# Optimization experiments

Hardware: AMD Instinct MI355X
Metric: run time of the kernel (lower is better)

Reference implementation:

```python
import jax, jax.numpy as jnp
import numpy as np

# config (matches init_kwargs)
B, H, N, D = 2, 8, 2048, 64
ALPHA = 1.0        # < 2 -> power-law kernel branch
D_INT = 4.0        # d_intrinsic
BW = 1.0           # bandwidth
A = 0.5            # dual-sided degree-normalization exponent
R = 1.0            # sphere_radius
MASK_VAL = 10000.0
EPS = 1e-7


def setup_inputs() -> dict:
    key = jax.random.key(0)
    k1, k2, k3, k4 = jax.random.split(key, 4)
    Q = jax.random.normal(k1, (B, H, N, D), dtype=jnp.float32)
    K = jax.random.normal(k2, (B, H, N, D), dtype=jnp.float32)
    V = jax.random.normal(k3, (B, H, N, D), dtype=jnp.float32)
    mask = jax.random.randint(k4, (B, N), 0, 2).astype(jnp.int32)
    return {"Q": Q, "K": K, "V": V, "mask": mask}


def reference(Q, K, V, mask) -> jnp.ndarray:
    # geodesic distance on the sphere: acos(clamp(QK^T)) * radius  [B,H,N,N]
    qk = jnp.einsum('bhnd,bhmd->bhnm', Q, K)
    g_dist = jnp.arccos(jnp.clip(qk, -1.0 + EPS, 1.0 - EPS)) * R
    # key-side padding mask: [B,N] -> [B,1,1,N]
    g_dist = jnp.where(mask[:, None, None, :] == 0, MASK_VAL, g_dist)
    # power-law kernel (alpha < 2 branch)
    attn_score = (1.0 + g_dist / jnp.sqrt(BW)) ** (-D_INT - ALPHA)
    # dual-sided degree normalization (a != 0 branch)
    n_r = jnp.sum(attn_score, axis=-1)   # row degrees [B,H,N]
    n_c = jnp.sum(attn_score, axis=-2)   # col degrees [B,H,N]
    k_tilde = (n_r ** (-A))[..., :, None] * attn_score * (n_c ** (-A))[..., None, :]
    # F.normalize(p=1, dim=3)
    attn = k_tilde / jnp.maximum(jnp.sum(jnp.abs(k_tilde), axis=-1, keepdims=True), 1e-12)
    # dropout p=0.0 -> identity
    return jnp.einsum('bhnm,bhmd->bhnd', attn, V)
```

## Files before the change

kernel.cpp:

```cpp
#include <hip/hip_runtime.h>
#include <hip/hip_bf16.h>
#include <math.h>

#define B_ 2
#define H_ 8
#define N_ 2048
#define D_ 64
#define BH_ 16
#define NT_ (N_/64)
#define LS 72
#define LSW (LS/2)

typedef __attribute__((ext_vector_type(8))) short short8;
typedef __attribute__((ext_vector_type(4))) float float4v;
typedef __attribute__((ext_vector_type(2))) float float2v;

__device__ __forceinline__ float2v splat2(float s){ float2v v; v.x=s; v.y=s; return v; }

__device__ __forceinline__ unsigned packbf2(float a, float b){
  __hip_bfloat162 h = __float22bfloat162_rn(make_float2(a, b));
  return *(unsigned*)&h;
}
__device__ __forceinline__ void split2(float a, float b, unsigned& hi, unsigned& lo){
  hi = packbf2(a, b);
  float ha = __uint_as_float(hi << 16);
  float hb = __uint_as_float(hi & 0xFFFF0000u);
  lo = packbf2(a - ha, b - hb);
}
__device__ __forceinline__ void load_split8(const float* p, short8& hi8, short8& lo8){
  float4v v0 = *(const float4v*)p;
  float4v v1 = *(const float4v*)(p + 4);
  unsigned h0,h1,h2,h3,l0,l1,l2,l3;
  split2(v0.x, v0.y, h0, l0);
  split2(v0.z, v0.w, h1, l1);
  split2(v1.x, v1.y, h2, l2);
  split2(v1.z, v1.w, h3, l3);
  unsigned ph[4] = {h0,h1,h2,h3};
  unsigned pl[4] = {l0,l1,l2,l3};
  hi8 = *(short8*)ph;
  lo8 = *(short8*)pl;
}

__device__ __forceinline__ float2v score2(float2v qk){
  float2v ax;
  ax.x = fminf(fabsf(qk.x), 1.0f - 1e-7f);
  ax.y = fminf(fabsf(qk.y), 1.0f - 1e-7f);
  float2v p = __builtin_elementwise_fma(
                __builtin_elementwise_fma(
                  __builtin_elementwise_fma(splat2(-0.0187293f), ax, splat2(0.0742610f)),
                  ax, splat2(-0.2121144f)),
                ax, splat2(1.5707288f));
  float2v u = __builtin_elementwise_fma(ax, splat2(-1.0f), splat2(1.0f));
  float2v t;
  t.x = __builtin_amdgcn_sqrtf(u.x);
  t.y = __builtin_amdgcn_sqrtf(u.y);
  float2v t2 = t * p;
  float2v gn = __builtin_elementwise_fma(t2, splat2(-1.0f), splat2(3.14159265358979f));
  float2v g;
  g.x = (qk.x >= 0.0f) ? t2.x : gn.x;
  g.y = (qk.y >= 0.0f) ? t2.y : gn.y;
  float2v w1 = g + splat2(1.0f);
  float2v w2 = w1 * w1;
  float2v w4 = w2 * w2;
  float2v w5 = w4 * w1;
  float2v r;
  r.x = __builtin_amdgcn_rcpf(w5.x);
  r.y = __builtin_amdgcn_rcpf(w5.y);
  return r;
}

__device__ __forceinline__ float score_fn_m(float qk, float masked){
  float ax = fminf(fabsf(qk), 1.0f - 1e-7f);
  float t  = __builtin_amdgcn_sqrtf(1.0f - ax);
  float p  = __builtin_fmaf(__builtin_fmaf(__builtin_fmaf(-0.0187293f, ax, 0.0742610f),
                                           ax, -0.2121144f), ax, 1.5707288f);
  float t2 = t * p;
  float g  = (qk >= 0.0f) ? t2 : (3.14159265358979f - t2);
  g = (masked != 0.0f) ? 10000.0f : g;
  float w1 = 1.0f + g;
  float w2 = w1*w1;
  float w4 = w2*w2;
  return __builtin_amdgcn_rcpf(w4*w1);
}

__global__ __launch_bounds__(256) void k0_split(
    const float* __restrict__ Q, const float* __restrict__ K,
    unsigned short* __restrict__ Qh, unsigned short* __restrict__ Ql,
    unsigned short* __restrict__ Kh, unsigned short* __restrict__ Kl)
{
  size_t i = (size_t)blockIdx.x*256 + threadIdx.x;
  const size_t tot = (size_t)BH_*N_*D_/8;
  const float* src; unsigned short *dh, *dl;
  if (i < tot){ src = Q; dh = Qh; dl = Ql; }
  else        { src = K; dh = Kh; dl = Kl; i -= tot; }
  short8 hi, lo;
  load_split8(src + i*8, hi, lo);
  *(short8*)&dh[i*8] = hi;
  *(short8*)&dl[i*8] = lo;
}

template<bool PRE>
__global__ __launch_bounds__(256) void k1_score(
    const float* __restrict__ Qf, const float* __restrict__ Kf,
    const unsigned short* __restrict__ Qh, const unsigned short* __restrict__ Ql,
    const unsigned short* __restrict__ Kh, const unsigned short* __restrict__ Kl,
    float* __restrict__ ncw, unsigned short* __restrict__ S)
{
  __shared__ float red[64*4];
  const int id = blockIdx.x;
  const int xcd = id & 7;
  const int r0 = id >> 3;
  const int kt = r0 & 31;
  const int grp = r0 >> 5;
  const int flat = grp*8 + xcd;
  const int bh = flat & 15;
  const int rz = flat >> 4;
  const int nz = 4;
  const int tid = threadIdx.x;
  const int wv = tid>>6, lane = tid&63, quad = lane>>4, l15 = lane&15;

  short8 khi[4][2], klo[4][2];
  if constexpr (PRE){
    #pragma unroll
    for (int s=0;s<4;++s){
      const size_t r = (size_t)(bh*N_ + kt*64 + s*16 + l15)*D_ + quad*8;
      khi[s][0] = *(const short8*)&Kh[r];
      khi[s][1] = *(const short8*)&Kh[r+32];
      klo[s][0] = *(const short8*)&Kl[r];
      klo[s][1] = *(const short8*)&Kl[r+32];
    }
  } else {
    #pragma unroll
    for (int s=0;s<4;++s){
      const float* kp = Kf + (size_t)(bh*N_ + kt*64 + s*16 + l15)*D_ + quad*8;
      load_split8(kp,      khi[s][0], klo[s][0]);
      load_split8(kp + 32, khi[s][1], klo[s][1]);
    }
  }

  float2v cs2[4][2];
  #pragma unroll
  for (int s=0;s<4;++s){ cs2[s][0] = splat2(0.f); cs2[s][1] = splat2(0.f); }

  const int iters = NT_/nz;
  const int rt0 = rz*iters;

  const size_t qoff0 = (size_t)(bh*N_ + rt0*64 + wv*16 + l15)*D_ + quad*8;
  const unsigned lconst = (unsigned)(((quad>>1)<<7) + (l15<<3) + ((quad&1)<<2));
  unsigned short* Sp = S + ((((size_t)(bh*NT_ + kt)*NT_ + rt0)*4 + wv)<<10) + lconst;

  short8 qh0,qh1,ql0,ql1;
  if constexpr (PRE){
    const unsigned short* qp = Qh + qoff0;
    const unsigned short* lp = Ql + qoff0;
    qh0 = *(const short8*)qp;      qh1 = *(const short8*)(qp+32);
    ql0 = *(const short8*)lp;      ql1 = *(const short8*)(lp+32);
  } else {
    const float* qp = Qf + qoff0;
    load_split8(qp,      qh0, ql0);
    load_split8(qp + 32, qh1, ql1);
  }

  for (int rti=0; rti<iters; ++rti){
    short8 nh0,nh1,nl0,nl1;
    const size_t qoffn = qoff0 + (size_t)(rti + ((rti+1<iters) ? 1 : 0))*4096;
    if constexpr (PRE){
      const unsigned short* qp = Qh + qoffn;
      const unsigned short* lp = Ql + qoffn;
      nh0 = *(const short8*)qp;    nh1 = *(const short8*)(qp+32);
      nl0 = *(const short8*)lp;    nl1 = *(const short8*)(lp+32);
    } else {
      const float* qp = Qf + qoffn;
      load_split8(qp,      nh0, nl0);
      load_split8(qp + 32, nh1, nl1);
    }

    #pragma unroll
    for (int s=0;s<4;++s){
      float4v c = {0.f,0.f,0.f,0.f};
      c = __builtin_amdgcn_mfma_f32_16x16x32_bf16(khi[s][0], qh0, c, 0,0,0);
      c = __builtin_amdgcn_mfma_f32_16x16x32_bf16(khi[s][0], ql0, c, 0,0,0);
      c = __builtin_amdgcn_mfma_f32_16x16x32_bf16(klo[s][0], qh0, c, 0,0,0);
      c = __builtin_amdgcn_mfma_f32_16x16x32_bf16(khi[s][1], qh1, c, 0,0,0);
      c = __builtin_amdgcn_mfma_f32_16x16x32_bf16(khi[s][1], ql1, c, 0,0,0);
      c = __builtin_amdgcn_mfma_f32_16x16x32_bf16(klo[s][1], qh1, c, 0,0,0);
      float2v c01; c01.x = c[0]; c01.y = c[1];
      float2v c23; c23.x = c[2]; c23.y = c[3];
      float2v s01 = score2(c01);
      float2v s23 = score2(c23);
      cs2[s][0] += s01;
      cs2[s][1] += s23;
      uint2 pk;
      pk.x = packbf2(s01.x, s01.y);
      pk.y = packbf2(s23.x, s23.y);
      *(uint2*)(Sp + (s<<8)) = pk;
    }
    Sp += 4096;
    qh0=nh0; qh1=nh1; ql0=nl0; ql1=nl1;
  }

  float cs[4][4];
  #pragma unroll
  for (int s=0;s<4;++s){
    cs[s][0]=cs2[s][0].x; cs[s][1]=cs2[s][0].y;
    cs[s][2]=cs2[s][1].x; cs[s][3]=cs2[s][1].y;
  }

  #pragma unroll
  for (int s=0;s<4;++s)
    #pragma unroll
    for (int i=0;i<4;++i){
      float v2 = cs[s][i];
      v2 += __shfl_xor(v2, 1);
      v2 += __shfl_xor(v2, 2);
      v2 += __shfl_xor(v2, 4);
      v2 += __shfl_xor(v2, 8);
      cs[s][i] = v2;
    }
  if (l15 == 0){
    #pragma unroll
    for (int s=0;s<4;++s)
      #pragma unroll
      for (int i=0;i<4;++i)
        red[(s*16 + quad*4 + i)*4 + wv] = cs[s][i];
  }
  __syncthreads();
  if (tid < 64){
    float t = red[tid*4+0] + red[tid*4+1] + red[tid*4+2] + red[tid*4+3];
    atomicAdd(&ncw[bh*N_ + kt*64 + tid], t);
  }
}

__global__ __launch_bounds__(256) void k2_pack(
    const float* __restrict__ V, const float* __restrict__ nc,
    const int* __restrict__ mask, unsigned short* __restrict__ Vw)
{
  __shared__ float T[64*65];
  __shared__ float wrow[64];
  const int mt = blockIdx.x, bh = blockIdx.y;
  const int tid = threadIdx.x;
  const float* Vg = V + (size_t)bh*N_*D_;
  const float* ncg = nc + (size_t)bh*N_;
  unsigned short* Fb = Vw + ((size_t)(bh*NT_ + mt)*10)*512;

  {
    int m = tid >> 2;
    int d0 = (tid & 3) * 16;
    int gm = mt*64 + m;
    float wm = (mask[(bh>>3)*N_ + gm] == 0) ? 0.0f
             : (1.0f / sqrtf(fmaxf(ncg[gm], 1e-30f)));
    if (d0 == 0) wrow[m] = wm;
    #pragma unroll
    for (int j=0;j<4;++j){
      float4v v = *(const float4v*)(Vg + (size_t)gm*D_ + d0 + j*4);
      T[(d0+j*4+0)*65 + m] = v.x*wm;
      T[(d0+j*4+1)*65 + m] = v.y*wm;
      T[(d0+j*4+2)*65 + m] = v.z*wm;
      T[(d0+j*4+3)*65 + m] = v.w*wm;
    }
  }
  __syncthreads();

  for (int idx = tid; idx < 640; idx += 256){
    int f = idx >> 6, lane = idx & 63;
    int quad = lane >> 4, l15 = lane & 15;
    int s2 = f >> 1, cc = f & 1;
    int m0 = cc*32 + quad*8;
    unsigned pk[4];
    if (s2 < 4){
      int d = s2*16 + l15;
      #pragma unroll
      for (int j=0;j<4;++j)
        pk[j] = packbf2(T[d*65 + m0 + 2*j], T[d*65 + m0 + 2*j + 1]);
    } else if (l15 == 0){
      #pragma unroll
      for (int j=0;j<4;++j)
        pk[j] = packbf2(wrow[m0 + 2*j], wrow[m0 + 2*j + 1]);
    } else {
      pk[0]=pk[1]=pk[2]=pk[3]=0u;
    }
    *(short8*)(Fb + ((size_t)f*64 + lane)*8) = *(short8*)pk;
  }
}

__global__ __launch_bounds__(512) void k3_direct(
    const unsigned short* __restrict__ S, const unsigned short* __restrict__ Vw,
    float* __restrict__ out)
{
  __shared__ float Red[64*68];

  const int id = blockIdx.x;
  const int xcd = id & 7;
  const int r0 = id >> 3;
  const int rt = r0 & 31;
  const int bhh = r0 >> 5;
  const int bh = bhh*8 + xcd;

  const int tid = threadIdx.x;
  const int wvid = tid >> 6;
  const int g    = wvid >> 2;
  const int slot = wvid & 3;
  const int lane = tid & 63, quad = lane >> 4, l15 = lane & 15;
  const int row = rt*64 + slot*16 + l15;

  const size_t sb0 = ((((size_t)bh*NT_ + g*16)*NT_ + rt)*4 + (size_t)slot)*1024
                   + (size_t)quad*128 + (size_t)l15*8;
  const unsigned short* Vb = Vw + ((size_t)(bh*NT_ + g*16)*10)*512 + (size_t)lane*8;

  float4v acc[4];
  #pragma unroll
  for (int i=0;i<4;++i) acc[i] = (float4v){0.f,0.f,0.f,0.f};
  float4v c5 = {0.f,0.f,0.f,0.f};

  short8 sA0 = *(const short8*)&S[sb0];
  short8 sA1 = *(const short8*)&S[sb0 + 512];
  short8 sB0 = *(const short8*)&S[sb0 + 131072];
  short8 sB1 = *(const short8*)&S[sb0 + 131072 + 512];

  #pragma unroll 1
  for (int k2 = 0; k2 < 8; ++k2){
    const int ktA = k2*2, ktB = k2*2 + 1;
    {
      const unsigned short* Vp = Vb + (size_t)ktA*5120;
      short8 va[10];
      #pragma unroll
      for (int f=0; f<10; ++f)
        va[f] = *(const short8*)(Vp + (size_t)f*512);
      short8 p0 = sA0, p1 = sA1;
      if (ktA + 2 < 16){
        const size_t sb = sb0 + (size_t)(ktA+2)*131072;
        sA0 = *(const short8*)&S[sb];
        sA1 = *(const short8*)&S[sb + 512];
      }
      #pragma unroll
      for (int s2=0;s2<4;++s2){
        acc[s2] = __builtin_amdgcn_mfma_f32_16x16x32_bf16(va[s2*2+0], p0, acc[s2], 0,0,0);
        acc[s2] = __builtin_amdgcn_mfma_f32_16x16x32_bf16(va[s2*2+1], p1, acc[s2], 0,0,0);
      }
      c5 = __builtin_amdgcn_mfma_f32_16x16x32_bf16(va[8], p0, c5, 0,0,0);
      c5 = __builtin_amdgcn_mfma_f32_16x16x32_bf16(va[9], p1, c5, 0,0,0);
    }
    {
      const unsigned short* Vp = Vb + (size_t)ktB*5120;
      short8 va[10];
      #pragma unroll
      for (int f=0; f<10; ++f)
        va[f] = *(const short8*)(Vp + (size_t)f*512);
      short8 p0 = sB0, p1 = sB1;
      if (ktB + 2 < 16){
        const size_t sb = sb0 + (size_t)(ktB+2)*131072;
        sB0 = *(const short8*)&S[sb];
        sB1 = *(const short8*)&S[sb + 512];
      }
      #pragma unroll
      for (int s2=0;s2<4;++s2){
        acc[s2] = __builtin_amdgcn_mfma_f32_16x16x32_bf16(va[s2*2+0], p0, acc[s2], 0,0,0);
        acc[s2] = __builtin_amdgcn_mfma_f32_16x16x32_bf16(va[s2*2+1], p1, acc[s2], 0,0,0);
      }
      c5 = __builtin_amdgcn_mfma_f32_16x16x32_bf16(va[8], p0, c5, 0,0,0);
      c5 = __builtin_amdgcn_mfma_f32_16x16x32_bf16(va[9], p1, c5, 0,0,0);
    }
  }

  if (g == 1){
    float* Rr = Red + (size_t)(slot*16 + l15)*68;
    #pragma unroll
    for (int s2=0;s2<4;++s2)
      #pragma unroll
      for (int i=0;i<4;++i)
        Rr[s2*16 + quad*4 + i] = acc[s2][i];
    if (quad == 0) Rr[64] = c5[0];
  }
  __syncthreads();
  if (g == 0){
    const float* Rr = Red + (size_t)(slot*16 + l15)*68;
    #pragma unroll
    for (int s2=0;s2<4;++s2)
      #pragma unroll
      for (int i=0;i<4;++i)
        acc[s2][i] += Rr[s2*16 + quad*4 + i];
    float rs = __shfl(c5[0], l15) + Rr[64];
    float inv = 1.0f / fmaxf(rs, 1e-12f);

    float* Og = out + (size_t)bh*N_*D_ + (size_t)row*D_;
    #pragma unroll
    for (int s2=0;s2<4;++s2)
      #pragma unroll
      for (int i=0;i<4;++i)
        Og[s2*16 + quad*4 + i] = acc[s2][i] * inv;
  }
}

__global__ __launch_bounds__(256) void k1_fallback(
    const float* __restrict__ Q, const float* __restrict__ K,
    const int* __restrict__ mask, float* __restrict__ ncw)
{
  __shared__ float msk[64];
  __shared__ float red[64*4];
  const int kt = blockIdx.x, bh = blockIdx.y;
  const int tid = threadIdx.x;
  const int wv = tid>>6, lane = tid&63, quad = lane>>4, l15 = lane&15;

  const float* Qg = Q + (size_t)bh*N_*D_;
  const float* Kg = K + (size_t)bh*N_*D_;

  short8 khi[4][2], klo[4][2];
  #pragma unroll
  for (int s=0;s<4;++s){
    const float* kp = Kg + (size_t)(kt*64 + s*16 + l15)*D_ + quad*8;
    load_split8(kp,      khi[s][0], klo[s][0]);
    load_split8(kp + 32, khi[s][1], klo[s][1]);
  }
  if (tid < 64)
    msk[tid] = (mask[(bh>>3)*N_ + kt*64 + tid] == 0) ? 1.f : 0.f;
  __syncthreads();

  float cs[4][4];
  #pragma unroll
  for (int s=0;s<4;++s)
    #pragma unroll
    for (int i=0;i<4;++i) cs[s][i] = 0.f;

  for (int rt=0; rt<NT_; ++rt){
    const float* qp = Qg + (size_t)(rt*64 + wv*16 + l15)*D_ + quad*8;
    short8 bhi[2], blo[2];
    load_split8(qp,      bhi[0], blo[0]);
    load_split8(qp + 32, bhi[1], blo[1]);

    #pragma unroll
    for (int s=0;s<4;++s){
      float4v c = {0.f,0.f,0.f,0.f};
      #pragma unroll
      for (int cc=0; cc<2; ++cc){
        c = __builtin_amdgcn_mfma_f32_16x16x32_bf16(khi[s][cc], bhi[cc], c, 0,0,0);
        c = __builtin_amdgcn_mfma_f32_16x16x32_bf16(khi[s][cc], blo[cc], c, 0,0,0);
        c = __builtin_amdgcn_mfma_f32_16x16x32_bf16(klo[s][cc], bhi[cc], c, 0,0,0);
      }
      int kl = s*16 + quad*4;
      cs[s][0] += score_fn_m(c[0], msk[kl+0]);
      cs[s][1] += score_fn_m(c[1], msk[kl+1]);
      cs[s][2] += score_fn_m(c[2], msk[kl+2]);
      cs[s][3] += score_fn_m(c[3], msk[kl+3]);
    }
  }

  #pragma unroll
  for (int s=0;s<4;++s)
    #pragma unroll
    for (int i=0;i<4;++i){
      float v2 = cs[s][i];
      v2 += __shfl_xor(v2, 1);
      v2 += __shfl_xor(v2, 2);
      v2 += __shfl_xor(v2, 4);
      v2 += __shfl_xor(v2, 8);
      cs[s][i] = v2;
    }
  if (l15 == 0){
    #pragma unroll
    for (int s=0;s<4;++s)
      #pragma unroll
      for (int i=0;i<4;++i)
        red[(s*16 + quad*4 + i)*4 + wv] = cs[s][i];
  }
  __syncthreads();
  if (tid < 64){
    float t = red[tid*4+0] + red[tid*4+1] + red[tid*4+2] + red[tid*4+3];
    ncw[bh*N_ + kt*64 + tid] = 1.0f / sqrtf(t);
  }
}

__global__ __launch_bounds__(256) void spop_pass2(
    const float* __restrict__ Q, const float* __restrict__ K,
    const float* __restrict__ V, const int* __restrict__ mask,
    const float* __restrict__ w, float* __restrict__ out)
{
  __shared__ unsigned short Khi[64*LS], Klo[64*LS];
  __shared__ unsigned short Vt[64*LS];
  __shared__ unsigned short Ps[64*LS];
  __shared__ float msk[64], wms[64];

  const int rt = blockIdx.x, bh = blockIdx.y, b = bh>>3;
  const int tid = threadIdx.x;
  const int wv = tid>>6, lane = tid&63, quad = lane>>4, l15 = lane&15;

  const float* Qg = Q + (size_t)bh*N_*D_;
  const float* Kg = K + (size_t)bh*N_*D_;
  const float* Vg = V + (size_t)bh*N_*D_;

  short8 qhi[2], qlo[2];
  {
    const float* qp = Qg + (size_t)(rt*64 + wv*16 + l15)*D_ + quad*8;
    load_split8(qp,      qhi[0], qlo[0]);
    load_split8(qp + 32, qhi[1], qlo[1]);
  }

  float4v acc[4];
  #pragma unroll
  for (int i=0;i<4;++i) acc[i] = (float4v){0.f,0.f,0.f,0.f};
  float rs = 0.f;

  for (int kt=0; kt<NT_; ++kt){
    __syncthreads();
    #pragma unroll
    for (int it=0; it<4; ++it){
      int idx = tid + it*256;
      int r = idx>>4, d4 = (idx&15)<<2;
      const float4v v = *(const float4v*)(Kg + (size_t)(kt*64 + r)*D_ + d4);
      unsigned h0,l0,h1,l1;
      split2(v.x, v.y, h0, l0);
      split2(v.z, v.w, h1, l1);
      unsigned* KhiW = (unsigned*)Khi; unsigned* KloW = (unsigned*)Klo;
      int base = r*LSW + (d4>>1);
      KhiW[base] = h0; KhiW[base+1] = h1;
      KloW[base] = l0; KloW[base+1] = l1;
    }
    #pragma unroll
    for (int it=0; it<2; ++it){
      int u = tid + it*256;
      int kp = u & 31;
      int d4 = (u>>5)<<2;
      const float* vp = Vg + (size_t)(kt*64 + kp*2)*D_ + d4;
      float4v a0 = *(const float4v*)vp;
      float4v a1 = *(const float4v*)(vp + D_);
      unsigned* VtW = (unsigned*)Vt;
      VtW[(d4+0)*LSW + kp] = packbf2(a0.x, a1.x);
      VtW[(d4+1)*LSW + kp] = packbf2(a0.y, a1.y);
      VtW[(d4+2)*LSW + kp] = packbf2(a0.z, a1.z);
      VtW[(d4+3)*LSW + kp] = packbf2(a0.w, a1.w);
    }
    if (tid < 64){
      int gk = kt*64 + tid;
      msk[tid] = (mask[b*N_ + gk] == 0) ? 1.f : 0.f;
      wms[tid] = w[bh*N_ + gk];
    }
    __syncthreads();

    #pragma unroll
    for (int s=0;s<4;++s){
      float4v c = {0.f,0.f,0.f,0.f};
      #pragma unroll
      for (int cc=0; cc<2; ++cc){
        const short8 ahi = *(const short8*)&Khi[(s*16+l15)*LS + cc*32 + quad*8];
        const short8 alo = *(const short8*)&Klo[(s*16+l15)*LS + cc*32 + quad*8];
        c = __builtin_amdgcn_mfma_f32_16x16x32_bf16(ahi, qhi[cc], c, 0,0,0);
        c = __builtin_amdgcn_mfma_f32_16x16x32_bf16(ahi, qlo[cc], c, 0,0,0);
        c = __builtin_amdgcn_mfma_f32_16x16x32_bf16(alo, qhi[cc], c, 0,0,0);
      }
      int kl = s*16 + quad*4;
      float sc0 = score_fn_m(c[0], msk[kl+0]) * wms[kl+0];
      float sc1 = score_fn_m(c[1], msk[kl+1]) * wms[kl+1];
      float sc2 = score_fn_m(c[2], msk[kl+2]) * wms[kl+2];
      float sc3 = score_fn_m(c[3], msk[kl+3]) * wms[kl+3];
      rs += (sc0 + sc1) + (sc2 + sc3);
      unsigned* PsW = (unsigned*)Ps;
      int pb = (wv*16 + l15)*LSW + (kl>>1);
      PsW[pb]   = packbf2(sc0, sc1);
      PsW[pb+1] = packbf2(sc2, sc3);
    }

    short8 pf[2];
    pf[0] = *(const short8*)&Ps[(wv*16+l15)*LS +  0 + quad*8];
    pf[1] = *(const short8*)&Ps[(wv*16+l15)*LS + 32 + quad*8];
    #pragma unroll
    for (int s2=0;s2<4;++s2){
      #pragma unroll
      for (int cc=0; cc<2; ++cc){
        const short8 av = *(const short8*)&Vt[(s2*16+l15)*LS + cc*32 + quad*8];
        acc[s2] = __builtin_amdgcn_mfma_f32_16x16x32_bf16(av, pf[cc], acc[s2], 0,0,0);
      }
    }
  }

  rs += __shfl_xor(rs, 16);
  rs += __shfl_xor(rs, 32);
  float inv = 1.0f / fmaxf(rs, 1e-12f);

  float* Og = out + (size_t)bh*N_*D_ + (size_t)(rt*64 + wv*16 + l15)*D_;
  #pragma unroll
  for (int s2=0;s2<4;++s2)
    #pragma unroll
    for (int i=0;i<4;++i)
      Og[s2*16 + quad*4 + i] = acc[s2][i] * inv;
}

extern "C" void kernel_launch(void* const* d_in, const int* in_sizes, int n_in,
                              void* d_out, int out_size, void* d_ws, size_t ws_size,
                              hipStream_t stream) {
  (void)in_sizes; (void)n_in; (void)out_size;
  const float* Q   = (const float*)d_in[0];
  const float* K   = (const float*)d_in[1];
  const float* V   = (const float*)d_in[2];
  const int*  mask = (const int*)d_in[3];
  float* out = (float*)d_out;

  const size_t nc_bytes = (size_t)BH_*N_*sizeof(float);
  const size_t vw_off   = 131072;
  const size_t vw_bytes = (size_t)BH_*NT_*10*512*2;
  const size_t qk_off   = vw_off + vw_bytes;
  const size_t qk_one   = (size_t)BH_*N_*D_;
  const size_t qk_bytes = 4*qk_one*2;
  const size_t S_bytes  = (size_t)2*BH_*N_*N_;
  const size_t need_A   = qk_off + qk_bytes + S_bytes;
  const size_t need_B   = qk_off + S_bytes;

  if (ws_size >= need_A){
    float* nc = (float*)d_ws;
    unsigned short* Vw = (unsigned short*)((char*)d_ws + vw_off);
    unsigned short* Qh = (unsigned short*)((char*)d_ws + qk_off);
    unsigned short* Ql = Qh + qk_one;
    unsigned short* Kh = Ql + qk_one;
    unsigned short* Kl = Kh + qk_one;
    unsigned short* S  = (unsigned short*)((char*)d_ws + qk_off + qk_bytes);
    hipMemsetAsync(nc, 0, nc_bytes, stream);
    k0_split<<<dim3(2048), 256, 0, stream>>>(Q, K, Qh, Ql, Kh, Kl);
    k1_score<true><<<dim3(2048), 256, 0, stream>>>(
        nullptr, nullptr, Qh, Ql, Kh, Kl, nc, S);
    k2_pack<<<dim3(NT_, BH_), 256, 0, stream>>>(V, nc, mask, Vw);
    k3_direct<<<dim3(512), 512, 0, stream>>>(S, Vw, out);
  } else if (ws_size >= need_B){
    float* nc = (float*)d_ws;
    unsigned short* Vw = (unsigned short*)((char*)d_ws + vw_off);
    unsigned short* S  = (unsigned short*)((char*)d_ws + qk_off);
    hipMemsetAsync(nc, 0, nc_bytes, stream);
    k1_score<false><<<dim3(2048), 256, 0, stream>>>(
        Q, K, nullptr, nullptr, nullptr, nullptr, nc, S);
    k2_pack<<<dim3(NT_, BH_), 256, 0, stream>>>(V, nc, mask, Vw);
    k3_direct<<<dim3(512), 512, 0, stream>>>(S, Vw, out);
  } else {
    float* w = (float*)d_ws;
    k1_fallback<<<dim3(NT_, BH_), 256, 0, stream>>>(Q, K, mask, w);
    spop_pass2<<<dim3(NT_, BH_), 256, 0, stream>>>(Q, K, V, mask, w, out);
  }
}
```

Measured before the change: 171.8 us.

## Re-tile score kernel so waves share Q rows, drop LDS reduction, nontemporal S

The score kernel now gives each block two key tiles, with each wave owning half a key tile (two 16-row slices). All four waves walk the same 16-row query chunks, so Q loads are shared across waves through cache and each wave holds fewer K registers. The shared-memory column-sum reduction and __syncthreads are replaced by direct per-wave atomicAdds, and the grid is halved. The score matrix is written and read with nontemporal stores and loads to avoid polluting cache, and launch bounds now request 4 blocks per CU. The cost is more global atomics and a different scheduling balance.

```diff
diff --git a/kernel.cpp b/kernel.cpp
--- a/kernel.cpp
+++ b/kernel.cpp
@@ -14,6 +14,7 @@
 typedef __attribute__((ext_vector_type(8))) short short8;
 typedef __attribute__((ext_vector_type(4))) float float4v;
 typedef __attribute__((ext_vector_type(2))) float float2v;
+typedef __attribute__((ext_vector_type(2))) unsigned int uint2v;
 
 __device__ __forceinline__ float2v splat2(float s){ float2v v; v.x=s; v.y=s; return v; }
 
@@ -100,134 +101,109 @@
 }
 
 template<bool PRE>
-__global__ __launch_bounds__(256) void k1_score(
+__global__ __launch_bounds__(256, 4) void k1_score(
     const float* __restrict__ Qf, const float* __restrict__ Kf,
     const unsigned short* __restrict__ Qh, const unsigned short* __restrict__ Ql,
     const unsigned short* __restrict__ Kh, const unsigned short* __restrict__ Kl,
     float* __restrict__ ncw, unsigned short* __restrict__ S)
 {
-  __shared__ float red[64*4];
   const int id = blockIdx.x;
   const int xcd = id & 7;
   const int r0 = id >> 3;
-  const int kt = r0 & 31;
-  const int grp = r0 >> 5;
+  const int kt2 = r0 & 15;
+  const int grp = r0 >> 4;
   const int flat = grp*8 + xcd;
   const int bh = flat & 15;
   const int rz = flat >> 4;
-  const int nz = 4;
   const int tid = threadIdx.x;
   const int wv = tid>>6, lane = tid&63, quad = lane>>4, l15 = lane&15;
-
-  short8 khi[4][2], klo[4][2];
-  if constexpr (PRE){
-    #pragma unroll
-    for (int s=0;s<4;++s){
-      const size_t r = (size_t)(bh*N_ + kt*64 + s*16 + l15)*D_ + quad*8;
-      khi[s][0] = *(const short8*)&Kh[r];
-      khi[s][1] = *(const short8*)&Kh[r+32];
-      klo[s][0] = *(const short8*)&Kl[r];
-      klo[s][1] = *(const short8*)&Kl[r+32];
-    }
-  } else {
-    #pragma unroll
-    for (int s=0;s<4;++s){
-      const float* kp = Kf + (size_t)(bh*N_ + kt*64 + s*16 + l15)*D_ + quad*8;
-      load_split8(kp,      khi[s][0], klo[s][0]);
-      load_split8(kp + 32, khi[s][1], klo[s][1]);
-    }
-  }
-
-  float2v cs2[4][2];
-  #pragma unroll
-  for (int s=0;s<4;++s){ cs2[s][0] = splat2(0.f); cs2[s][1] = splat2(0.f); }
-
-  const int iters = NT_/nz;
-  const int rt0 = rz*iters;
-
-  const size_t qoff0 = (size_t)(bh*N_ + rt0*64 + wv*16 + l15)*D_ + quad*8;
+  const int kt  = kt2*2 + (wv>>1);
+  const int sb2 = (wv&1)*2;
+
+  short8 khi[2][2], klo[2][2];
+  #pragma unroll
+  for (int sl=0; sl<2; ++sl){
+    const size_t r = (size_t)(bh*N_ + kt*64 + (sb2+sl)*16 + l15)*D_ + quad*8;
+    if constexpr (PRE){
+      khi[sl][0] = *(const short8*)&Kh[r];
+      khi[sl][1] = *(const short8*)&Kh[r+32];
+      klo[sl][0] = *(const short8*)&Kl[r];
+      klo[sl][1] = *(const short8*)&Kl[r+32];
+    } else {
+      load_split8(Kf + r,      khi[sl][0], klo[sl][0]);
+      load_split8(Kf + r + 32, khi[sl][1], klo[sl][1]);
+    }
+  }
+
+  float2v cs2[2][2];
+  #pragma unroll
+  for (int sl=0;sl<2;++sl){ cs2[sl][0] = splat2(0.f); cs2[sl][1] = splat2(0.f); }
+
+  const int iters = 32;
+  const int m0 = rz*32;
+
+  size_t qoff0 = (size_t)(bh*N_ + m0*16 + l15)*D_ + quad*8;
   const unsigned lconst = (unsigned)(((quad>>1)<<7) + (l15<<3) + ((quad&1)<<2));
-  unsigned short* Sp = S + ((((size_t)(bh*NT_ + kt)*NT_ + rt0)*4 + wv)<<10) + lconst;
+  unsigned short* Sp = S + (((size_t)(bh*NT_ + kt)*128 + (unsigned)m0)<<10)
+                         + (unsigned)(sb2<<8) + lconst;
 
   short8 qh0,qh1,ql0,ql1;
   if constexpr (PRE){
-    const unsigned short* qp = Qh + qoff0;
-    const unsigned short* lp = Ql + qoff0;
-    qh0 = *(const short8*)qp;      qh1 = *(const short8*)(qp+32);
-    ql0 = *(const short8*)lp;      ql1 = *(const short8*)(lp+32);
+    qh0 = *(const short8*)&Qh[qoff0];  qh1 = *(const short8*)&Qh[qoff0+32];
+    ql0 = *(const short8*)&Ql[qoff0];  ql1 = *(const short8*)&Ql[qoff0+32];
   } else {
-    const float* qp = Qf + qoff0;
-    load_split8(qp,      qh0, ql0);
-    load_split8(qp + 32, qh1, ql1);
+    load_split8(Qf + qoff0,      qh0, ql0);
+    load_split8(Qf + qoff0 + 32, qh1, ql1);
   }
 
   for (int rti=0; rti<iters; ++rti){
     short8 nh0,nh1,nl0,nl1;
-    const size_t qoffn = qoff0 + (size_t)(rti + ((rti+1<iters) ? 1 : 0))*4096;
+    const size_t qoffn = qoff0 + (size_t)(rti + ((rti+1<iters) ? 1 : 0))*1024;
     if constexpr (PRE){
-      const unsigned short* qp = Qh + qoffn;
-      const unsigned short* lp = Ql + qoffn;
-      nh0 = *(const short8*)qp;    nh1 = *(const short8*)(qp+32);
-      nl0 = *(const short8*)lp;    nl1 = *(const short8*)(lp+32);
+      nh0 = *(const short8*)&Qh[qoffn];  nh1 = *(const short8*)&Qh[qoffn+32];
+      nl0 = *(const short8*)&Ql[qoffn];  nl1 = *(const short8*)&Ql[qoffn+32];
     } else {
-      const float* qp = Qf + qoffn;
-      load_split8(qp,      nh0, nl0);
-      load_split8(qp + 32, nh1, nl1);
-    }
-
-    #pragma unroll
-    for (int s=0;s<4;++s){
+      load_split8(Qf + qoffn,      nh0, nl0);
+      load_split8(Qf + qoffn + 32, nh1, nl1);
+    }
+
+    #pragma unroll
+    for (int sl=0; sl<2; ++sl){
       float4v c = {0.f,0.f,0.f,0.f};
-      c = __builtin_amdgcn_mfma_f32_16x16x32_bf16(khi[s][0], qh0, c, 0,0,0);
-      c = __builtin_amdgcn_mfma_f32_16x16x32_bf16(khi[s][0], ql0, c, 0,0,0);
-      c = __builtin_amdgcn_mfma_f32_16x16x32_bf16(klo[s][0], qh0, c, 0,0,0);
-      c = __builtin_amdgcn_mfma_f32_16x16x32_bf16(khi[s][1], qh1, c, 0,0,0);
-      c = __builtin_amdgcn_mfma_f32_16x16x32_bf16(khi[s][1], ql1, c, 0,0,0);
-      c = __builtin_amdgcn_mfma_f32_16x16x32_bf16(klo[s][1], qh1, c, 0,0,0);
+      c = __builtin_amdgcn_mfma_f32_16x16x32_bf16(khi[sl][0], qh0, c, 0,0,0);
+      c = __builtin_amdgcn_mfma_f32_16x16x32_bf16(khi[sl][0], ql0, c, 0,0,0);
+      c = __builtin_amdgcn_mfma_f32_16x16x32_bf16(klo[sl][0], qh0, c, 0,0,0);
+      c = __builtin_amdgcn_mfma_f32_16x16x32_bf16(khi[sl][1], qh1, c, 0,0,0);
+      c = __builtin_amdgcn_mfma_f32_16x16x32_bf16(khi[sl][1], ql1, c, 0,0,0);
+      c = __builtin_amdgcn_mfma_f32_16x16x32_bf16(klo[sl][1], qh1, c, 0,0,0);
       float2v c01; c01.x = c[0]; c01.y = c[1];
       float2v c23; c23.x = c[2]; c23.y = c[3];
       float2v s01 = score2(c01);
       float2v s23 = score2(c23);
-      cs2[s][0] += s01;
-      cs2[s][1] += s23;
-      uint2 pk;
+      cs2[sl][0] += s01;
+      cs2[sl][1] += s23;
+      uint2v pk;
       pk.x = packbf2(s01.x, s01.y);
       pk.y = packbf2(s23.x, s23.y);
-      *(uint2*)(Sp + (s<<8)) = pk;
-    }
-    Sp += 4096;
+      __builtin_nontemporal_store(pk, (uint2v*)(Sp + (sl<<8)));
+    }
+    Sp += 1024;
     qh0=nh0; qh1=nh1; ql0=nl0; ql1=nl1;
   }
 
-  float cs[4][4];
-  #pragma unroll
-  for (int s=0;s<4;++s){
-    cs[s][0]=cs2[s][0].x; cs[s][1]=cs2[s][0].y;
-    cs[s][2]=cs2[s][1].x; cs[s][3]=cs2[s][1].y;
-  }
-
-  #pragma unroll
-  for (int s=0;s<4;++s)
+  #pragma unroll
+  for (int sl=0; sl<2; ++sl){
+    float cs[4] = {cs2[sl][0].x, cs2[sl][0].y, cs2[sl][1].x, cs2[sl][1].y};
     #pragma unroll
     for (int i=0;i<4;++i){
-      float v2 = cs[s][i];
+      float v2 = cs[i];
       v2 += __shfl_xor(v2, 1);
       v2 += __shfl_xor(v2, 2);
       v2 += __shfl_xor(v2, 4);
       v2 += __shfl_xor(v2, 8);
-      cs[s][i] = v2;
-    }
-  if (l15 == 0){
-    #pragma unroll
-    for (int s=0;s<4;++s)
-      #pragma unroll
-      for (int i=0;i<4;++i)
-        red[(s*16 + quad*4 + i)*4 + wv] = cs[s][i];
-  }
-  __syncthreads();
-  if (tid < 64){
-    float t = red[tid*4+0] + red[tid*4+1] + red[tid*4+2] + red[tid*4+3];
-    atomicAdd(&ncw[bh*N_ + kt*64 + tid], t);
+      if (l15 == 0)
+        atomicAdd(&ncw[bh*N_ + kt*64 + (sb2+sl)*16 + quad*4 + i], v2);
+    }
   }
 }
 
@@ -312,10 +288,10 @@
   for (int i=0;i<4;++i) acc[i] = (float4v){0.f,0.f,0.f,0.f};
   float4v c5 = {0.f,0.f,0.f,0.f};
 
-  short8 sA0 = *(const short8*)&S[sb0];
-  short8 sA1 = *(const short8*)&S[sb0 + 512];
-  short8 sB0 = *(const short8*)&S[sb0 + 131072];
-  short8 sB1 = *(const short8*)&S[sb0 + 131072 + 512];
+  short8 sA0 = __builtin_nontemporal_load((const short8*)&S[sb0]);
+  short8 sA1 = __builtin_nontemporal_load((const short8*)&S[sb0 + 512]);
+  short8 sB0 = __builtin_nontemporal_load((const short8*)&S[sb0 + 131072]);
+  short8 sB1 = __builtin_nontemporal_load((const short8*)&S[sb0 + 131072 + 512]);
 
   #pragma unroll 1
   for (int k2 = 0; k2 < 8; ++k2){
@@ -329,8 +305,8 @@
       short8 p0 = sA0, p1 = sA1;
       if (ktA + 2 < 16){
         const size_t sb = sb0 + (size_t)(ktA+2)*131072;
-        sA0 = *(const short8*)&S[sb];
-        sA1 = *(const short8*)&S[sb + 512];
+        sA0 = __builtin_nontemporal_load((const short8*)&S[sb]);
+        sA1 = __builtin_nontemporal_load((const short8*)&S[sb + 512]);
       }
       #pragma unroll
       for (int s2=0;s2<4;++s2){
@@ -349,8 +325,8 @@
       short8 p0 = sB0, p1 = sB1;
       if (ktB + 2 < 16){
         const size_t sb = sb0 + (size_t)(ktB+2)*131072;
-        sB0 = *(const short8*)&S[sb];
-        sB1 = *(const short8*)&S[sb + 512];
+        sB0 = __builtin_nontemporal_load((const short8*)&S[sb]);
+        sB1 = __builtin_nontemporal_load((const short8*)&S[sb + 512]);
       }
       #pragma unroll
       for (int s2=0;s2<4;++s2){
@@ -613,7 +589,7 @@
     unsigned short* S  = (unsigned short*)((char*)d_ws + qk_off + qk_bytes);
     hipMemsetAsync(nc, 0, nc_bytes, stream);
     k0_split<<<dim3(2048), 256, 0, stream>>>(Q, K, Qh, Ql, Kh, Kl);
-    k1_score<true><<<dim3(2048), 256, 0, stream>>>(
+    k1_score<true><<<dim3(1024), 256, 0, stream>>>(
         nullptr, nullptr, Qh, Ql, Kh, Kl, nc, S);
     k2_pack<<<dim3(NT_, BH_), 256, 0, stream>>>(V, nc, mask, Vw);
     k3_direct<<<dim3(512), 512, 0, stream>>>(S, Vw, out);
@@ -622,7 +598,7 @@
     unsigned short* Vw = (unsigned short*)((char*)d_ws + vw_off);
     unsigned short* S  = (unsigned short*)((char*)d_ws + qk_off);
     hipMemsetAsync(nc, 0, nc_bytes, stream);
-    k1_score<false><<<dim3(2048), 256, 0, stream>>>(
+    k1_score<false><<<dim3(1024), 256, 0, stream>>>(
         Q, K, nullptr, nullptr, nullptr, nullptr, nc, S);
     k2_pack<<<dim3(NT_, BH_), 256, 0, stream>>>(V, nc, mask, Vw);
     k3_direct<<<dim3(512), 512, 0, stream>>>(S, Vw, out);
```

Result: slower. 191.4 us (+11.4%).
